# Performance work log

Hardware: AMD Instinct MI355X
Metric: run time of the kernel (lower is better)

## Reference

```python
import jax, jax.numpy as jnp
import numpy as np
import math

B, N, M = 8, 16384, 64
D_LAT, D_COORD, H = 256, 2, 256
NUM_LAYERS = 4          # -> NUM_LAYERS+1 Gabor filters
T_CHUNK, C_OUT = 16, 2
FREQ = T_CHUNK // 2 + 1
OUT_DIM = FREQ * 2 * C_OUT  # 36
N_HEADS, HEAD_DIM = 8, D_LAT // 8


def setup_inputs() -> dict:
    key = jax.random.key(0)
    ks = iter(jax.random.split(key, 40))
    nf = NUM_LAYERS + 1
    ws = 256.0 / math.sqrt(nf)
    gamma = jax.random.uniform(next(ks), (nf, H), minval=0.1, maxval=2.0)
    gabor_W = jax.random.normal(next(ks), (nf, H, D_COORD)) * (ws / math.sqrt(D_COORD)) * jnp.sqrt(gamma)[..., None]
    gabor_b = jax.random.uniform(next(ks), (nf, H), minval=-math.pi, maxval=math.pi)
    gabor_mu = jax.random.uniform(next(ks), (nf, H, D_COORD), minval=-1.0, maxval=1.0)
    u = lambda k, sh, d: jax.random.uniform(k, sh, minval=-math.sqrt(1.0 / d), maxval=math.sqrt(1.0 / d))
    net1_W = u(next(ks), (NUM_LAYERS, H, H), H)
    net1_b = u(next(ks), (NUM_LAYERS, H), H)
    net2_W = u(next(ks), (nf, H, D_LAT), D_LAT)
    qp_W1 = u(next(ks), (H, D_COORD), D_COORD); qp_b1 = u(next(ks), (H,), D_COORD)
    qp_W2 = u(next(ks), (D_LAT, H), H); qp_b2 = u(next(ks), (D_LAT,), H)
    in_W = u(next(ks), (3 * D_LAT, D_LAT), D_LAT); in_b = jnp.zeros((3 * D_LAT,))
    out_W = u(next(ks), (D_LAT, D_LAT), D_LAT); out_b = jnp.zeros((D_LAT,))
    lnq_g = jnp.ones((D_LAT,)); lnq_b = jnp.zeros((D_LAT,))
    lnkv_g = jnp.ones((D_LAT,)); lnkv_b = jnp.zeros((D_LAT,))
    fin_W = u(next(ks), (OUT_DIM, H), H); fin_b = u(next(ks), (OUT_DIM,), H)
    z_multi = jax.random.normal(next(ks), (B, M, D_LAT), dtype=jnp.float32)
    coords = jax.random.uniform(next(ks), (B, N, D_COORD), dtype=jnp.float32)
    return dict(z_multi=z_multi, coords=coords, gabor_W=gabor_W, gabor_b=gabor_b,
                gabor_mu=gabor_mu, gabor_gamma=gamma, net1_W=net1_W, net1_b=net1_b,
                net2_W=net2_W, qp_W1=qp_W1, qp_b1=qp_b1, qp_W2=qp_W2, qp_b2=qp_b2,
                in_W=in_W, in_b=in_b, out_W=out_W, out_b=out_b,
                lnq_g=lnq_g, lnq_b=lnq_b, lnkv_g=lnkv_g, lnkv_b=lnkv_b,
                fin_W=fin_W, fin_b=fin_b)


def _layernorm(x, g, b, eps=1e-5):
    mu = x.mean(-1, keepdims=True)
    var = ((x - mu) ** 2).mean(-1, keepdims=True)
    return (x - mu) * jax.lax.rsqrt(var + eps) * g + b


def _gabor(x0, W, b, mu, gamma):
    # x0: [B,N,2], W: [H,2], mu: [H,2], gamma: [H]
    D = ((x0 ** 2).sum(-1)[..., None] + (mu ** 2).sum(-1)[None, None, :]
         - 2.0 * jnp.einsum('bnc,hc->bnh', x0, mu))
    return jnp.sin(jnp.einsum('bnc,hc->bnh', x0, W) + b) * jnp.exp(-0.5 * D * gamma)


def reference(z_multi, coords, gabor_W, gabor_b, gabor_mu, gabor_gamma,
              net1_W, net1_b, net2_W, qp_W1, qp_b1, qp_W2, qp_b2,
              in_W, in_b, out_W, out_b, lnq_g, lnq_b, lnkv_g, lnkv_b,
              fin_W, fin_b):
    x0 = coords  # use_node_type=False
    # query_proj: Linear -> GELU(exact) -> Linear
    q = jax.nn.gelu(jnp.einsum('bnc,hc->bnh', x0, qp_W1) + qp_b1, approximate=False)
    q = jnp.einsum('bnh,dh->bnd', q, qp_W2) + qp_b2
    q = _layernorm(q, lnq_g, lnq_b)
    kv = _layernorm(z_multi, lnkv_g, lnkv_b)
    # multihead cross-attention (torch nn.MultiheadAttention semantics)
    Wq, Wk, Wv = jnp.split(in_W, 3, axis=0)
    bq, bk, bv = jnp.split(in_b, 3, axis=0)
    Q = (jnp.einsum('bnd,ed->bne', q, Wq) + bq).reshape(B, N, N_HEADS, HEAD_DIM)
    K = (jnp.einsum('bmd,ed->bme', kv, Wk) + bk).reshape(B, M, N_HEADS, HEAD_DIM)
    V = (jnp.einsum('bmd,ed->bme', kv, Wv) + bv).reshape(B, M, N_HEADS, HEAD_DIM)
    scores = jnp.einsum('bnhk,bmhk->bhnm', Q, K) / math.sqrt(HEAD_DIM)
    attn = jax.nn.softmax(scores, axis=-1)
    ctx = jnp.einsum('bhnm,bmhk->bnhk', attn, V).reshape(B, N, D_LAT)
    z = jnp.einsum('bnd,ed->bne', ctx, out_W) + out_b
    # MFN Gabor loop
    x = _gabor(x0, gabor_W[0], gabor_b[0], gabor_mu[0], gabor_gamma[0]) \
        * jnp.einsum('bnd,hd->bnh', z, net2_W[0])
    for i in range(1, NUM_LAYERS + 1):
        basis = _gabor(x0, gabor_W[i], gabor_b[i], gabor_mu[i], gabor_gamma[i])
        h = (jnp.einsum('bnh,gh->bng', x, net1_W[i - 1]) + net1_b[i - 1]
             + jnp.einsum('bnd,hd->bnh', z, net2_W[i]))
        x = basis * h
    out = jnp.einsum('bnh,oh->bno', x, fin_W) + fin_b  # [B,N,36]
    # FFT head: view as complex freq coeffs and inverse rfft over time axis
    fr = out.reshape(B, N, FREQ, C_OUT, 2).transpose(0, 2, 1, 3, 4)  # [B,F,N,C,2]
    fc = fr[..., 0] + 1j * fr[..., 1]
    return jnp.fft.irfft(fc, n=T_CHUNK, axis=1, norm='ortho')  # [B,16,N,2]
```

## Files before the change

kernel.cpp:

```cpp
#include <hip/hip_runtime.h>
#include <math.h>

#define NTOT 131072

typedef unsigned short ushort_t;
typedef __attribute__((ext_vector_type(8))) short short8;
typedef __attribute__((ext_vector_type(4))) float f32x4;

__device__ __forceinline__ float bf2f(ushort_t u){
  unsigned int v = ((unsigned int)u) << 16; float f;
  __builtin_memcpy(&f, &v, 4); return f;
}
__device__ __forceinline__ ushort_t f2bf(float f){
  unsigned int x; __builtin_memcpy(&x, &f, 4);
  x = (x + 0x7fffu + ((x >> 16) & 1u)) >> 16;
  return (ushort_t)x;
}
__device__ __forceinline__ void gld16(const void* g, void* l){
  __builtin_amdgcn_global_load_lds((const __attribute__((address_space(1))) void*)g,
                                   (__attribute__((address_space(3))) void*)l, 16, 0, 0);
}

__global__ __launch_bounds__(256) void packhl_k(const float* __restrict__ src, ushort_t* __restrict__ dst, int n){
  int i = blockIdx.x*256 + threadIdx.x;
  if (i < n){
    float v = src[i];
    ushort_t hi = f2bf(v);
    dst[i] = hi;
    dst[n + i] = f2bf(v - bf2f(hi));
  }
}

__global__ __launch_bounds__(256) void prepkv_f(const float* __restrict__ zm, const float* __restrict__ inW,
    const float* __restrict__ inb, const float* __restrict__ g, const float* __restrict__ bv,
    float* __restrict__ Kf, float* __restrict__ Vf){
  __shared__ float zr[256];
  __shared__ float red[256];
  int bm = blockIdx.x;
  int t = threadIdx.x;
  float v = zm[(size_t)bm*256 + t];
  red[t] = v; __syncthreads();
  for (int s = 128; s > 0; s >>= 1){ if (t < s) red[t] += red[t+s]; __syncthreads(); }
  float mu = red[0] * (1.f/256.f); __syncthreads();
  red[t] = (v-mu)*(v-mu); __syncthreads();
  for (int s = 128; s > 0; s >>= 1){ if (t < s) red[t] += red[t+s]; __syncthreads(); }
  float var = red[0] * (1.f/256.f);
  float rsd = rsqrtf(var + 1e-5f);
  __syncthreads();
  zr[t] = (v - mu) * rsd * g[t] + bv[t];
  __syncthreads();
  float accK = inb[256+t], accV = inb[512+t];
  const float* wk = inW + (size_t)(256+t)*256;
  const float* wv = inW + (size_t)(512+t)*256;
  for (int d = 0; d < 256; d += 4){
    float4 a = *(const float4*)(zr + d);
    float4 k4 = *(const float4*)(wk + d);
    float4 v4 = *(const float4*)(wv + d);
    accK += a.x*k4.x + a.y*k4.y + a.z*k4.z + a.w*k4.w;
    accV += a.x*v4.x + a.y*v4.y + a.z*v4.z + a.w*v4.w;
  }
  Kf[(size_t)bm*256 + t] = accK;
  Vf[(size_t)bm*256 + t] = accV;
}

__global__ __launch_bounds__(256) void hidden_f(const float* __restrict__ coords, const float* __restrict__ W1,
    const float* __restrict__ b1, float* __restrict__ out, int pt0){
  int h = threadIdx.x; int p0 = blockIdx.x*4;
  float w0 = W1[h*2], w1 = W1[h*2+1], bb = b1[h];
  #pragma unroll
  for (int pp = 0; pp < 4; ++pp){
    size_t gpt = (size_t)(pt0 + p0 + pp);
    float x = coords[gpt*2], y = coords[gpt*2+1];
    float v = x*w0 + y*w1 + bb;
    out[(size_t)(p0+pp)*256 + h] = 0.5f * v * (1.f + erff(v * 0.70710678118654752f));
  }
}

__device__ __forceinline__ void stage_w32(const ushort_t* Wbase, int oc, ushort_t* dsth, ushort_t* dstl, int w, int lane){
  #pragma unroll
  for (int part = 0; part < 2; ++part){
    const char* src0 = (const char*)(Wbase + part*65536);
    char* dst = (char*)(part ? dstl : dsth);
    #pragma unroll
    for (int i = 0; i < 4; ++i){
      int flat = ((w*4+i)*64 + lane)*16;
      int row = flat >> 9, kb = flat & 511;
      int skb = kb ^ ((row & 31) << 4);
      gld16(src0 + (size_t)(oc*32+row)*512 + skb, dst + (size_t)(w*4+i)*1024);
    }
  }
}

__device__ __forceinline__ void split_frags(const float* Ar, short8* ah, short8* al, int q4){
  #pragma unroll
  for (int kc = 0; kc < 8; ++kc){
    const float* p = Ar + kc*32 + q4*8;
    short8 h8, l8;
    #pragma unroll
    for (int j = 0; j < 8; ++j){
      float v = p[j];
      ushort_t hi = f2bf(v);
      h8[j] = (short)hi;
      l8[j] = (short)f2bf(v - bf2f(hi));
    }
    ah[kc] = h8; al[kc] = l8;
  }
}

template<int EPI, int NPASS>
__global__ __launch_bounds__(256) void gemm3f_k(const float* __restrict__ A0,
    const float* __restrict__ A1, const ushort_t* __restrict__ W0,
    const ushort_t* __restrict__ W1, const float* __restrict__ bias,
    const float* __restrict__ lng, const float* __restrict__ lnb,
    const float* __restrict__ coords, const float* __restrict__ gW,
    const float* __restrict__ gb, const float* __restrict__ gmu,
    const float* __restrict__ gg, int pt0g, int fidx,
    float* __restrict__ outp){
  __shared__ ushort_t Whs[2][32*256];
  __shared__ ushort_t Wls[2][32*256];
  const int tid = threadIdx.x, lane = tid & 63, w = tid >> 6;
  const int r16 = lane & 15, q4 = lane >> 4;
  const int row0 = blockIdx.x * 64;
  const size_t arow = (size_t)(row0 + w*16 + r16);

  short8 ah[8], al[8];
  split_frags(A0 + arow*256, ah, al, q4);
  stage_w32(W0, 0, Whs[0], Wls[0], w, lane);

  f32x4 acc[16];
  #pragma unroll
  for (int i = 0; i < 16; ++i) acc[i] = (f32x4){0.f,0.f,0.f,0.f};
  __syncthreads();

  constexpr int TCH = NPASS*8;
  for (int t = 0; t < TCH; ++t){
    const int buf = t & 1;
    if (t + 1 < TCH){
      const int tn = t + 1;
      stage_w32((tn >= 8) ? W1 : W0, tn & 7, Whs[tn&1], Wls[tn&1], w, lane);
    }
    if constexpr (NPASS == 2){
      if (t == 8) split_frags(A1 + arow*256, ah, al, q4);
    }
    const int oc = t & 7;
    const char* Bh = (const char*)Whs[buf];
    const char* Bl = (const char*)Wls[buf];
    #pragma unroll
    for (int kc = 0; kc < 8; ++kc){
      const int koff = (kc*32 + q4*8)*2;
      #pragma unroll
      for (int cg = 0; cg < 2; ++cg){
        const int wrow = cg*16 + r16;
        const int off = koff ^ ((wrow & 31) << 4);
        short8 bh = *(const short8*)(Bh + (size_t)wrow*512 + off);
        short8 bl = *(const short8*)(Bl + (size_t)wrow*512 + off);
        f32x4 a_ = acc[oc*2+cg];
        a_ = __builtin_amdgcn_mfma_f32_16x16x32_bf16(ah[kc], bh, a_, 0, 0, 0);
        a_ = __builtin_amdgcn_mfma_f32_16x16x32_bf16(al[kc], bh, a_, 0, 0, 0);
        a_ = __builtin_amdgcn_mfma_f32_16x16x32_bf16(ah[kc], bl, a_, 0, 0, 0);
        acc[oc*2+cg] = a_;
      }
    }
    __syncthreads();
  }

  const int crow = row0 + w*16 + q4*4;
  if (bias){
    #pragma unroll
    for (int idx = 0; idx < 16; ++idx){
      const int col = (idx>>1)*32 + (idx&1)*16 + r16;
      const float bb = bias[col];
      #pragma unroll
      for (int r = 0; r < 4; ++r) acc[idx][r] += bb;
    }
  }
  if constexpr (EPI == 1){
    float mu[4], rs[4];
    #pragma unroll
    for (int r = 0; r < 4; ++r){
      float s = 0.f, s2 = 0.f;
      #pragma unroll
      for (int idx = 0; idx < 16; ++idx){ float v = acc[idx][r]; s += v; s2 += v*v; }
      #pragma unroll
      for (int m = 1; m < 16; m <<= 1){ s += __shfl_xor(s, m); s2 += __shfl_xor(s2, m); }
      float mean = s * (1.f/256.f);
      float var = s2 * (1.f/256.f) - mean*mean;
      mu[r] = mean; rs[r] = rsqrtf(var + 1e-5f);
    }
    #pragma unroll
    for (int idx = 0; idx < 16; ++idx){
      const int col = (idx>>1)*32 + (idx&1)*16 + r16;
      const float gv = lng[col], bv = lnb[col];
      #pragma unroll
      for (int r = 0; r < 4; ++r)
        outp[(size_t)(crow + r)*256 + col] = (acc[idx][r] - mu[r]) * rs[r] * gv + bv;
    }
  } else if constexpr (EPI == 2){
    float xs[4], ys[4], xx[4];
    #pragma unroll
    for (int r = 0; r < 4; ++r){
      size_t gp = (size_t)(pt0g + crow + r);
      float x = coords[gp*2], y = coords[gp*2+1];
      xs[r] = x; ys[r] = y; xx[r] = x*x + y*y;
    }
    #pragma unroll
    for (int idx = 0; idx < 16; ++idx){
      const int col = (idx>>1)*32 + (idx&1)*16 + r16;
      const int o = fidx*256 + col;
      const float w0 = gW[o*2], w1 = gW[o*2+1];
      const float m0 = gmu[o*2], m1 = gmu[o*2+1];
      const float bb = gb[o], ga = gg[o];
      const float mm = m0*m0 + m1*m1;
      #pragma unroll
      for (int r = 0; r < 4; ++r){
        float D = xx[r] + mm - 2.f*(xs[r]*m0 + ys[r]*m1);
        float bas = sinf(xs[r]*w0 + ys[r]*w1 + bb) * expf(-0.5f * D * ga);
        outp[(size_t)(crow + r)*256 + col] = acc[idx][r] * bas;
      }
    }
  } else {
    #pragma unroll
    for (int idx = 0; idx < 16; ++idx){
      const int col = (idx>>1)*32 + (idx&1)*16 + r16;
      #pragma unroll
      for (int r = 0; r < 4; ++r)
        outp[(size_t)(crow + r)*256 + col] = acc[idx][r];
    }
  }
}

__global__ __launch_bounds__(512) void attn3_k(const float* __restrict__ Q,
    const float* __restrict__ Kf, const float* __restrict__ Vf,
    float* __restrict__ ctx, int pt0){
  __shared__ float Kl[64*256];
  __shared__ float Vl[64*256];
  const int tid = threadIdx.x;
  const int p = tid & 63, h = tid >> 6;
  const int prow0 = blockIdx.x * 64;
  const int b = (pt0 + prow0) >> 14;
  {
    const float4* Kg = (const float4*)(Kf + (size_t)b*64*256);
    const float4* Vg = (const float4*)(Vf + (size_t)b*64*256);
    float4* Klv = (float4*)Kl;
    float4* Vlv = (float4*)Vl;
    #pragma unroll
    for (int i = 0; i < 8; ++i){
      int ix = i*512 + tid;
      Klv[ix] = Kg[ix];
      Vlv[ix] = Vg[ix];
    }
  }
  __syncthreads();

  const size_t qrow = (size_t)(prow0 + p)*256 + h*32;
  const float scale = 0.17677669529663687f;
  float q[32];
  #pragma unroll
  for (int k4 = 0; k4 < 32; k4 += 4){
    float4 qv = *(const float4*)(Q + qrow + k4);
    q[k4] = qv.x; q[k4+1] = qv.y; q[k4+2] = qv.z; q[k4+3] = qv.w;
  }
  float mx = -1e30f;
  #pragma unroll 4
  for (int m = 0; m < 64; ++m){
    const float* Kr = Kl + m*256 + h*32;
    float s = 0.f;
    #pragma unroll
    for (int k4 = 0; k4 < 32; k4 += 4){
      float4 kv = *(const float4*)(Kr + k4);
      s += q[k4]*kv.x + q[k4+1]*kv.y + q[k4+2]*kv.z + q[k4+3]*kv.w;
    }
    mx = fmaxf(mx, s*scale);
  }
  float o[32];
  #pragma unroll
  for (int d = 0; d < 32; ++d) o[d] = 0.f;
  float sum = 0.f;
  #pragma unroll 2
  for (int m = 0; m < 64; ++m){
    const float* Kr = Kl + m*256 + h*32;
    float s = 0.f;
    #pragma unroll
    for (int k4 = 0; k4 < 32; k4 += 4){
      float4 kv = *(const float4*)(Kr + k4);
      s += q[k4]*kv.x + q[k4+1]*kv.y + q[k4+2]*kv.z + q[k4+3]*kv.w;
    }
    float pe = __expf(s*scale - mx);
    sum += pe;
    const float* Vr = Vl + m*256 + h*32;
    #pragma unroll
    for (int d4 = 0; d4 < 32; d4 += 4){
      float4 vv = *(const float4*)(Vr + d4);
      o[d4] += pe*vv.x; o[d4+1] += pe*vv.y; o[d4+2] += pe*vv.z; o[d4+3] += pe*vv.w;
    }
  }
  const float inv = 1.f / sum;
  #pragma unroll
  for (int d4 = 0; d4 < 32; d4 += 4){
    float4 ov;
    ov.x = o[d4]*inv; ov.y = o[d4+1]*inv; ov.z = o[d4+2]*inv; ov.w = o[d4+3]*inv;
    *(float4*)(ctx + qrow + d4) = ov;
  }
}

__global__ __launch_bounds__(256) void fin_f(const float* __restrict__ X, const float* __restrict__ fW,
    const float* __restrict__ fb, float* __restrict__ outp, int pt0){
  __shared__ float Xl[64][260];
  __shared__ float s36p[64][4][37];
  __shared__ float ctab[7][16];
  __shared__ float stab[7][16];
  const int tid = threadIdx.x;
  const int row0 = blockIdx.x * 64;
  if (tid < 112){
    int f = tid >> 4, t = tid & 15;
    float a = 3.14159265358979323846f * (float)((f+1)*t) / 8.f;
    float s, c; sincosf(a, &s, &c);
    ctab[f][t] = c; stab[f][t] = s;
  }
  #pragma unroll
  for (int i = 0; i < 16; ++i){
    int r = i*4 + (tid >> 6);
    *(float4*)(&Xl[r][(tid&63)*4]) = *(const float4*)(X + (size_t)(row0 + r)*256 + (tid&63)*4);
  }
  __syncthreads();
  {
    const int p = tid & 63, g = tid >> 6;
    float xs[64];
    #pragma unroll
    for (int k4 = 0; k4 < 64; k4 += 4){
      float4 xv = *(const float4*)(&Xl[p][g*64 + k4]);
      xs[k4] = xv.x; xs[k4+1] = xv.y; xs[k4+2] = xv.z; xs[k4+3] = xv.w;
    }
    #pragma unroll
    for (int c = 0; c < 36; ++c){
      const float* Wr = fW + (size_t)c*256 + g*64;
      float s = 0.f;
      #pragma unroll
      for (int k4 = 0; k4 < 64; k4 += 4){
        float4 wv = *(const float4*)(Wr + k4);
        s += xs[k4]*wv.x + xs[k4+1]*wv.y + xs[k4+2]*wv.z + xs[k4+3]*wv.w;
      }
      s36p[p][g][c] = s;
    }
  }
  __syncthreads();

  const int pl = tid & 63, tg = tid >> 6;
  const int gpt = pt0 + row0 + pl;
  const int b = gpt >> 14; const int n = gpt & 16383;
  float R[36];
  #pragma unroll
  for (int i = 0; i < 36; ++i)
    R[i] = s36p[pl][0][i] + s36p[pl][1][i] + s36p[pl][2][i] + s36p[pl][3][i] + fb[i];
  #pragma unroll
  for (int tt = 0; tt < 4; ++tt){
    int t = tg*4 + tt;
    float o0 = 0.f, o1 = 0.f;
    #pragma unroll
    for (int c = 0; c < 2; ++c){
      float v = R[c*2] + ((t & 1) ? -R[32 + c*2] : R[32 + c*2]);
      #pragma unroll
      for (int f = 1; f < 8; ++f){
        v += 2.f * (R[f*4 + c*2] * ctab[f-1][t] - R[f*4 + c*2 + 1] * stab[f-1][t]);
      }
      v *= 0.25f;
      if (c == 0) o0 = v; else o1 = v;
    }
    float2 wv; wv.x = o0; wv.y = o1;
    *(float2*)(outp + ((size_t)(b*16 + t)*16384 + n)*2) = wv;
  }
}

extern "C" void kernel_launch(void* const* d_in, const int* in_sizes, int n_in,
                              void* d_out, int out_size, void* d_ws, size_t ws_size,
                              hipStream_t stream){
  const float* z_multi=(const float*)d_in[0];
  const float* coords =(const float*)d_in[1];
  const float* gW =(const float*)d_in[2];
  const float* gb =(const float*)d_in[3];
  const float* gmu=(const float*)d_in[4];
  const float* gg =(const float*)d_in[5];
  const float* n1W=(const float*)d_in[6];
  const float* n1b=(const float*)d_in[7];
  const float* n2W=(const float*)d_in[8];
  const float* qpW1=(const float*)d_in[9];
  const float* qpb1=(const float*)d_in[10];
  const float* qpW2=(const float*)d_in[11];
  const float* qpb2=(const float*)d_in[12];
  const float* inW=(const float*)d_in[13];
  const float* inb=(const float*)d_in[14];
  const float* outW=(const float*)d_in[15];
  const float* outb=(const float*)d_in[16];
  const float* lnqg=(const float*)d_in[17];
  const float* lnqb=(const float*)d_in[18];
  const float* lnkg=(const float*)d_in[19];
  const float* lnkb=(const float*)d_in[20];
  const float* finW=(const float*)d_in[21];
  const float* finb=(const float*)d_in[22];
  float* outp=(float*)d_out;
  char* ws=(char*)d_ws;

  ushort_t* Wqp2=(ushort_t*)(ws + 0);
  ushort_t* Wq  =(ushort_t*)(ws + 262144);
  ushort_t* Wout=(ushort_t*)(ws + 524288);
  ushort_t* Wn2 =(ushort_t*)(ws + 786432);
  ushort_t* Wn1 =(ushort_t*)(ws + 2097152);
  float* Kf = (float*)(ws + 3145728);
  float* Vf = (float*)(ws + 3670016);
  const size_t BASE = 4194304;
  size_t avail = (ws_size > BASE) ? (ws_size - BASE) : 0;
  long long ncl = (long long)(avail / 3072) & ~127LL;
  if (ncl < 128) ncl = 128;
  if (ncl > NTOT) ncl = NTOT;
  const int NC = (int)ncl;
  float* S0 = (float*)(ws + BASE);
  float* S1 = S0 + (size_t)NC*256;
  float* S2 = S1 + (size_t)NC*256;

  packhl_k<<<256,256,0,stream>>>(qpW2, Wqp2, 65536);
  packhl_k<<<256,256,0,stream>>>(inW,  Wq,   65536);
  packhl_k<<<256,256,0,stream>>>(outW, Wout, 65536);
  for (int l = 0; l < 5; ++l)
    packhl_k<<<256,256,0,stream>>>(n2W + (size_t)l*65536, Wn2 + (size_t)l*131072, 65536);
  for (int l = 0; l < 4; ++l)
    packhl_k<<<256,256,0,stream>>>(n1W + (size_t)l*65536, Wn1 + (size_t)l*131072, 65536);
  prepkv_f<<<512,256,0,stream>>>(z_multi, inW, inb, lnkg, lnkb, Kf, Vf);

  for (int pt0 = 0; pt0 < NTOT; pt0 += NC){
    int nc = NTOT - pt0; if (nc > NC) nc = NC;
    int nb64 = nc / 64, np4 = nc / 4;
    hidden_f<<<np4,256,0,stream>>>(coords, qpW1, qpb1, S0, pt0);
    gemm3f_k<1,1><<<nb64,256,0,stream>>>(S0, nullptr, Wqp2, nullptr, qpb2, lnqg, lnqb,
                                         nullptr, nullptr, nullptr, nullptr, nullptr, 0, 0, S1);
    gemm3f_k<0,1><<<nb64,256,0,stream>>>(S1, nullptr, Wq, nullptr, inb, nullptr, nullptr,
                                         nullptr, nullptr, nullptr, nullptr, nullptr, 0, 0, S2);
    attn3_k<<<nb64,512,0,stream>>>(S2, Kf, Vf, S0, pt0);
    gemm3f_k<0,1><<<nb64,256,0,stream>>>(S0, nullptr, Wout, nullptr, outb, nullptr, nullptr,
                                         nullptr, nullptr, nullptr, nullptr, nullptr, 0, 0, S1);
    gemm3f_k<2,1><<<nb64,256,0,stream>>>(S1, nullptr, Wn2, nullptr, nullptr, nullptr, nullptr,
                                         coords, gW, gb, gmu, gg, pt0, 0, S0);
    float* xa = S0; float* xb = S2;
    for (int i = 1; i <= 4; ++i){
      gemm3f_k<2,2><<<nb64,256,0,stream>>>(xa, S1, Wn1 + (size_t)(i-1)*131072, Wn2 + (size_t)i*131072,
                                           n1b + (size_t)(i-1)*256, nullptr, nullptr,
                                           coords, gW, gb, gmu, gg, pt0, i, xb);
      float* tmp = xa; xa = xb; xb = tmp;
    }
    fin_f<<<nb64,256,0,stream>>>(xa, finW, finb, outp, pt0);
  }
}
```

Baseline: 2.611 ms.

## Store intermediate activations as pre-split bf16 hi/lo pairs across all stages

Every producer kernel (hidden, GEMM epilogues, attention) now writes activations as bf16 hi and lo halves in a 512-wide row, not fp32. Consumer GEMMs load those halves straight into MFMA fragments and skip the per-block float-to-bf16 split. The attention kernel also drops V from LDS, reads V from global memory, and splits the QK dot product across four partial accumulators. The byte footprint per element is unchanged, so the saving comes from removing split arithmetic on the GEMM load side, at the cost of the split moving into every epilogue as strided 2-byte stores.

```diff
diff --git a/kernel.cpp b/kernel.cpp
--- a/kernel.cpp
+++ b/kernel.cpp
@@ -5,6 +5,7 @@
 
 typedef unsigned short ushort_t;
 typedef __attribute__((ext_vector_type(8))) short short8;
+typedef __attribute__((ext_vector_type(4))) short short4_t;
 typedef __attribute__((ext_vector_type(4))) float f32x4;
 
 __device__ __forceinline__ float bf2f(ushort_t u){
@@ -19,6 +20,11 @@
 __device__ __forceinline__ void gld16(const void* g, void* l){
   __builtin_amdgcn_global_load_lds((const __attribute__((address_space(1))) void*)g,
                                    (__attribute__((address_space(3))) void*)l, 16, 0, 0);
+}
+__device__ __forceinline__ void store_hl(ushort_t* row, int col, float v){
+  ushort_t hi = f2bf(v);
+  row[col] = hi;
+  row[col + 256] = f2bf(v - bf2f(hi));
 }
 
 __global__ __launch_bounds__(256) void packhl_k(const float* __restrict__ src, ushort_t* __restrict__ dst, int n){
@@ -63,8 +69,8 @@
   Vf[(size_t)bm*256 + t] = accV;
 }
 
-__global__ __launch_bounds__(256) void hidden_f(const float* __restrict__ coords, const float* __restrict__ W1,
-    const float* __restrict__ b1, float* __restrict__ out, int pt0){
+__global__ __launch_bounds__(256) void hidden_h(const float* __restrict__ coords, const float* __restrict__ W1,
+    const float* __restrict__ b1, ushort_t* __restrict__ out, int pt0){
   int h = threadIdx.x; int p0 = blockIdx.x*4;
   float w0 = W1[h*2], w1 = W1[h*2+1], bb = b1[h];
   #pragma unroll
@@ -72,7 +78,8 @@
     size_t gpt = (size_t)(pt0 + p0 + pp);
     float x = coords[gpt*2], y = coords[gpt*2+1];
     float v = x*w0 + y*w1 + bb;
-    out[(size_t)(p0+pp)*256 + h] = 0.5f * v * (1.f + erff(v * 0.70710678118654752f));
+    float gl = 0.5f * v * (1.f + erff(v * 0.70710678118654752f));
+    store_hl(out + (size_t)(p0+pp)*512, h, gl);
   }
 }
 
@@ -91,31 +98,23 @@
   }
 }
 
-__device__ __forceinline__ void split_frags(const float* Ar, short8* ah, short8* al, int q4){
+__device__ __forceinline__ void load_frags(const ushort_t* Ar, short8* ah, short8* al, int q4){
   #pragma unroll
   for (int kc = 0; kc < 8; ++kc){
-    const float* p = Ar + kc*32 + q4*8;
-    short8 h8, l8;
-    #pragma unroll
-    for (int j = 0; j < 8; ++j){
-      float v = p[j];
-      ushort_t hi = f2bf(v);
-      h8[j] = (short)hi;
-      l8[j] = (short)f2bf(v - bf2f(hi));
-    }
-    ah[kc] = h8; al[kc] = l8;
+    ah[kc] = *(const short8*)(Ar + kc*32 + q4*8);
+    al[kc] = *(const short8*)(Ar + 256 + kc*32 + q4*8);
   }
 }
 
 template<int EPI, int NPASS>
-__global__ __launch_bounds__(256) void gemm3f_k(const float* __restrict__ A0,
-    const float* __restrict__ A1, const ushort_t* __restrict__ W0,
+__global__ __launch_bounds__(256) void gemm4_k(const ushort_t* __restrict__ A0,
+    const ushort_t* __restrict__ A1, const ushort_t* __restrict__ W0,
     const ushort_t* __restrict__ W1, const float* __restrict__ bias,
     const float* __restrict__ lng, const float* __restrict__ lnb,
     const float* __restrict__ coords, const float* __restrict__ gW,
     const float* __restrict__ gb, const float* __restrict__ gmu,
     const float* __restrict__ gg, int pt0g, int fidx,
-    float* __restrict__ outp){
+    ushort_t* __restrict__ outp){
   __shared__ ushort_t Whs[2][32*256];
   __shared__ ushort_t Wls[2][32*256];
   const int tid = threadIdx.x, lane = tid & 63, w = tid >> 6;
@@ -124,7 +123,7 @@
   const size_t arow = (size_t)(row0 + w*16 + r16);
 
   short8 ah[8], al[8];
-  split_frags(A0 + arow*256, ah, al, q4);
+  load_frags(A0 + arow*512, ah, al, q4);
   stage_w32(W0, 0, Whs[0], Wls[0], w, lane);
 
   f32x4 acc[16];
@@ -140,7 +139,7 @@
       stage_w32((tn >= 8) ? W1 : W0, tn & 7, Whs[tn&1], Wls[tn&1], w, lane);
     }
     if constexpr (NPASS == 2){
-      if (t == 8) split_frags(A1 + arow*256, ah, al, q4);
+      if (t == 8) load_frags(A1 + arow*512, ah, al, q4);
     }
     const int oc = t & 7;
     const char* Bh = (const char*)Whs[buf];
@@ -192,8 +191,10 @@
       const int col = (idx>>1)*32 + (idx&1)*16 + r16;
       const float gv = lng[col], bv = lnb[col];
       #pragma unroll
-      for (int r = 0; r < 4; ++r)
-        outp[(size_t)(crow + r)*256 + col] = (acc[idx][r] - mu[r]) * rs[r] * gv + bv;
+      for (int r = 0; r < 4; ++r){
+        float v = (acc[idx][r] - mu[r]) * rs[r] * gv + bv;
+        store_hl(outp + (size_t)(crow + r)*512, col, v);
+      }
     }
   } else if constexpr (EPI == 2){
     float xs[4], ys[4], xx[4];
@@ -215,7 +216,7 @@
       for (int r = 0; r < 4; ++r){
         float D = xx[r] + mm - 2.f*(xs[r]*m0 + ys[r]*m1);
         float bas = sinf(xs[r]*w0 + ys[r]*w1 + bb) * expf(-0.5f * D * ga);
-        outp[(size_t)(crow + r)*256 + col] = acc[idx][r] * bas;
+        store_hl(outp + (size_t)(crow + r)*512, col, acc[idx][r] * bas);
       }
     }
   } else {
@@ -224,54 +225,58 @@
       const int col = (idx>>1)*32 + (idx&1)*16 + r16;
       #pragma unroll
       for (int r = 0; r < 4; ++r)
-        outp[(size_t)(crow + r)*256 + col] = acc[idx][r];
-    }
-  }
-}
-
-__global__ __launch_bounds__(512) void attn3_k(const float* __restrict__ Q,
+        store_hl(outp + (size_t)(crow + r)*512, col, acc[idx][r]);
+    }
+  }
+}
+
+__global__ __launch_bounds__(512) void attn4_k(const ushort_t* __restrict__ Q2,
     const float* __restrict__ Kf, const float* __restrict__ Vf,
-    float* __restrict__ ctx, int pt0){
+    ushort_t* __restrict__ ctx, int pt0){
   __shared__ float Kl[64*256];
-  __shared__ float Vl[64*256];
   const int tid = threadIdx.x;
   const int p = tid & 63, h = tid >> 6;
   const int prow0 = blockIdx.x * 64;
   const int b = (pt0 + prow0) >> 14;
   {
     const float4* Kg = (const float4*)(Kf + (size_t)b*64*256);
-    const float4* Vg = (const float4*)(Vf + (size_t)b*64*256);
     float4* Klv = (float4*)Kl;
-    float4* Vlv = (float4*)Vl;
     #pragma unroll
     for (int i = 0; i < 8; ++i){
       int ix = i*512 + tid;
       Klv[ix] = Kg[ix];
-      Vlv[ix] = Vg[ix];
-    }
-  }
-  __syncthreads();
-
-  const size_t qrow = (size_t)(prow0 + p)*256 + h*32;
+    }
+  }
+  __syncthreads();
+
+  const ushort_t* Qr = Q2 + (size_t)(prow0 + p)*512 + h*32;
   const float scale = 0.17677669529663687f;
   float q[32];
   #pragma unroll
-  for (int k4 = 0; k4 < 32; k4 += 4){
-    float4 qv = *(const float4*)(Q + qrow + k4);
-    q[k4] = qv.x; q[k4+1] = qv.y; q[k4+2] = qv.z; q[k4+3] = qv.w;
+  for (int g = 0; g < 4; ++g){
+    short8 h8 = *(const short8*)(Qr + g*8);
+    short8 l8 = *(const short8*)(Qr + 256 + g*8);
+    #pragma unroll
+    for (int j = 0; j < 8; ++j)
+      q[g*8+j] = bf2f((ushort_t)h8[j]) + bf2f((ushort_t)l8[j]);
   }
   float mx = -1e30f;
-  #pragma unroll 4
+  #pragma unroll 2
   for (int m = 0; m < 64; ++m){
     const float* Kr = Kl + m*256 + h*32;
-    float s = 0.f;
-    #pragma unroll
-    for (int k4 = 0; k4 < 32; k4 += 4){
-      float4 kv = *(const float4*)(Kr + k4);
-      s += q[k4]*kv.x + q[k4+1]*kv.y + q[k4+2]*kv.z + q[k4+3]*kv.w;
-    }
+    float ss0=0.f, ss1=0.f, ss2=0.f, ss3=0.f;
+    #pragma unroll
+    for (int k4 = 0; k4 < 8; ++k4){
+      float4 kv = *(const float4*)(Kr + k4*4);
+      const float* qq = q + k4*4;
+      float d = qq[0]*kv.x + qq[1]*kv.y + qq[2]*kv.z + qq[3]*kv.w;
+      if ((k4 & 3) == 0) ss0 += d; else if ((k4 & 3) == 1) ss1 += d;
+      else if ((k4 & 3) == 2) ss2 += d; else ss3 += d;
+    }
+    float s = (ss0 + ss1) + (ss2 + ss3);
     mx = fmaxf(mx, s*scale);
   }
+  const float* Vb = Vf + (size_t)b*64*256 + h*32;
   float o[32];
   #pragma unroll
   for (int d = 0; d < 32; ++d) o[d] = 0.f;
@@ -279,15 +284,19 @@
   #pragma unroll 2
   for (int m = 0; m < 64; ++m){
     const float* Kr = Kl + m*256 + h*32;
-    float s = 0.f;
-    #pragma unroll
-    for (int k4 = 0; k4 < 32; k4 += 4){
-      float4 kv = *(const float4*)(Kr + k4);
-      s += q[k4]*kv.x + q[k4+1]*kv.y + q[k4+2]*kv.z + q[k4+3]*kv.w;
-    }
+    float ss0=0.f, ss1=0.f, ss2=0.f, ss3=0.f;
+    #pragma unroll
+    for (int k4 = 0; k4 < 8; ++k4){
+      float4 kv = *(const float4*)(Kr + k4*4);
+      const float* qq = q + k4*4;
+      float d = qq[0]*kv.x + qq[1]*kv.y + qq[2]*kv.z + qq[3]*kv.w;
+      if ((k4 & 3) == 0) ss0 += d; else if ((k4 & 3) == 1) ss1 += d;
+      else if ((k4 & 3) == 2) ss2 += d; else ss3 += d;
+    }
+    float s = (ss0 + ss1) + (ss2 + ss3);
     float pe = __expf(s*scale - mx);
     sum += pe;
-    const float* Vr = Vl + m*256 + h*32;
+    const float* Vr = Vb + (size_t)m*256;
     #pragma unroll
     for (int d4 = 0; d4 < 32; d4 += 4){
       float4 vv = *(const float4*)(Vr + d4);
@@ -295,15 +304,17 @@
     }
   }
   const float inv = 1.f / sum;
-  #pragma unroll
-  for (int d4 = 0; d4 < 32; d4 += 4){
-    float4 ov;
-    ov.x = o[d4]*inv; ov.y = o[d4+1]*inv; ov.z = o[d4+2]*inv; ov.w = o[d4+3]*inv;
-    *(float4*)(ctx + qrow + d4) = ov;
-  }
-}
-
-__global__ __launch_bounds__(256) void fin_f(const float* __restrict__ X, const float* __restrict__ fW,
+  ushort_t* Cr = ctx + (size_t)(prow0 + p)*512 + h*32;
+  #pragma unroll
+  for (int d = 0; d < 32; ++d){
+    float cv = o[d]*inv;
+    ushort_t hi = f2bf(cv);
+    Cr[d] = hi;
+    Cr[d + 256] = f2bf(cv - bf2f(hi));
+  }
+}
+
+__global__ __launch_bounds__(256) void fin_h(const ushort_t* __restrict__ X, const float* __restrict__ fW,
     const float* __restrict__ fb, float* __restrict__ outp, int pt0){
   __shared__ float Xl[64][260];
   __shared__ float s36p[64][4][37];
@@ -320,7 +331,16 @@
   #pragma unroll
   for (int i = 0; i < 16; ++i){
     int r = i*4 + (tid >> 6);
-    *(float4*)(&Xl[r][(tid&63)*4]) = *(const float4*)(X + (size_t)(row0 + r)*256 + (tid&63)*4);
+    int c4 = (tid & 63)*4;
+    const ushort_t* Xr = X + (size_t)(row0 + r)*512 + c4;
+    short4_t h4 = *(const short4_t*)(Xr);
+    short4_t l4 = *(const short4_t*)(Xr + 256);
+    float4 v;
+    v.x = bf2f((ushort_t)h4[0]) + bf2f((ushort_t)l4[0]);
+    v.y = bf2f((ushort_t)h4[1]) + bf2f((ushort_t)l4[1]);
+    v.z = bf2f((ushort_t)h4[2]) + bf2f((ushort_t)l4[2]);
+    v.w = bf2f((ushort_t)h4[3]) + bf2f((ushort_t)l4[3]);
+    *(float4*)(&Xl[r][c4]) = v;
   }
   __syncthreads();
   {
@@ -413,9 +433,9 @@
   if (ncl < 128) ncl = 128;
   if (ncl > NTOT) ncl = NTOT;
   const int NC = (int)ncl;
-  float* S0 = (float*)(ws + BASE);
-  float* S1 = S0 + (size_t)NC*256;
-  float* S2 = S1 + (size_t)NC*256;
+  ushort_t* S0 = (ushort_t*)(ws + BASE);
+  ushort_t* S1 = S0 + (size_t)NC*512;
+  ushort_t* S2 = S1 + (size_t)NC*512;
 
   packhl_k<<<256,256,0,stream>>>(qpW2, Wqp2, 65536);
   packhl_k<<<256,256,0,stream>>>(inW,  Wq,   65536);
@@ -429,23 +449,23 @@
   for (int pt0 = 0; pt0 < NTOT; pt0 += NC){
     int nc = NTOT - pt0; if (nc > NC) nc = NC;
     int nb64 = nc / 64, np4 = nc / 4;
-    hidden_f<<<np4,256,0,stream>>>(coords, qpW1, qpb1, S0, pt0);
-    gemm3f_k<1,1><<<nb64,256,0,stream>>>(S0, nullptr, Wqp2, nullptr, qpb2, lnqg, lnqb,
-                                         nullptr, nullptr, nullptr, nullptr, nullptr, 0, 0, S1);
-    gemm3f_k<0,1><<<nb64,256,0,stream>>>(S1, nullptr, Wq, nullptr, inb, nullptr, nullptr,
-                                         nullptr, nullptr, nullptr, nullptr, nullptr, 0, 0, S2);
-    attn3_k<<<nb64,512,0,stream>>>(S2, Kf, Vf, S0, pt0);
-    gemm3f_k<0,1><<<nb64,256,0,stream>>>(S0, nullptr, Wout, nullptr, outb, nullptr, nullptr,
-                                         nullptr, nullptr, nullptr, nullptr, nullptr, 0, 0, S1);
-    gemm3f_k<2,1><<<nb64,256,0,stream>>>(S1, nullptr, Wn2, nullptr, nullptr, nullptr, nullptr,
-                                         coords, gW, gb, gmu, gg, pt0, 0, S0);
-    float* xa = S0; float* xb = S2;
+    hidden_h<<<np4,256,0,stream>>>(coords, qpW1, qpb1, S0, pt0);
+    gemm4_k<1,1><<<nb64,256,0,stream>>>(S0, nullptr, Wqp2, nullptr, qpb2, lnqg, lnqb,
+                                        nullptr, nullptr, nullptr, nullptr, nullptr, 0, 0, S1);
+    gemm4_k<0,1><<<nb64,256,0,stream>>>(S1, nullptr, Wq, nullptr, inb, nullptr, nullptr,
+                                        nullptr, nullptr, nullptr, nullptr, nullptr, 0, 0, S2);
+    attn4_k<<<nb64,512,0,stream>>>(S2, Kf, Vf, S0, pt0);
+    gemm4_k<0,1><<<nb64,256,0,stream>>>(S0, nullptr, Wout, nullptr, outb, nullptr, nullptr,
+                                        nullptr, nullptr, nullptr, nullptr, nullptr, 0, 0, S1);
+    gemm4_k<2,1><<<nb64,256,0,stream>>>(S1, nullptr, Wn2, nullptr, nullptr, nullptr, nullptr,
+                                        coords, gW, gb, gmu, gg, pt0, 0, S0);
+    ushort_t* xa = S0; ushort_t* xb = S2;
     for (int i = 1; i <= 4; ++i){
-      gemm3f_k<2,2><<<nb64,256,0,stream>>>(xa, S1, Wn1 + (size_t)(i-1)*131072, Wn2 + (size_t)i*131072,
-                                           n1b + (size_t)(i-1)*256, nullptr, nullptr,
-                                           coords, gW, gb, gmu, gg, pt0, i, xb);
-      float* tmp = xa; xa = xb; xb = tmp;
-    }
-    fin_f<<<nb64,256,0,stream>>>(xa, finW, finb, outp, pt0);
-  }
-}
+      gemm4_k<2,2><<<nb64,256,0,stream>>>(xa, S1, Wn1 + (size_t)(i-1)*131072, Wn2 + (size_t)i*131072,
+                                          n1b + (size_t)(i-1)*256, nullptr, nullptr,
+                                          coords, gW, gb, gmu, gg, pt0, i, xb);
+      ushort_t* tmp = xa; xa = xb; xb = tmp;
+    }
+    fin_h<<<nb64,256,0,stream>>>(xa, finW, finb, outp, pt0);
+  }
+}
```

Result: slower. 3.332 ms (+27.6%).
